# Performance work log

Hardware: AMD Instinct MI355X
Metric: run time of the kernel (lower is better)

## Reference

```python
import jax, jax.numpy as jnp
import numpy as np

NUM_DIM = 384
NUM_HEADS = 12
WIN = 7
L = WIN * WIN
NW = 4
B_ = 1024

def _relative_coords():
    ch, cw = np.meshgrid(np.arange(WIN), np.arange(WIN), indexing='ij')
    coords = np.stack([ch, cw]).reshape(2, -1)  # (2, L)
    rel = coords[:, :, None] - coords[:, None, :]  # (2, L, L)
    rel[0] += WIN - 1
    rel[1] += WIN - 1
    rel[0] *= 2 * WIN - 1
    return jnp.asarray(rel.sum(0), dtype=jnp.int32)  # (L, L)

def setup_inputs() -> dict:
    key = jax.random.key(0)
    k_x, k_m, k_qkv, k_pw, k_pb, k_rb = jax.random.split(key, 6)
    x = jax.random.normal(k_x, (B_, L, NUM_DIM), dtype=jnp.float32)
    mask = jax.random.bernoulli(k_m, 0.5, (NW, L, L))
    qkv_w = jax.random.normal(k_qkv, (3 * NUM_DIM, NUM_DIM), dtype=jnp.float32) * (NUM_DIM ** -0.5)
    proj_w = jax.random.normal(k_pw, (NUM_DIM, NUM_DIM), dtype=jnp.float32) * (NUM_DIM ** -0.5)
    proj_b = jax.random.normal(k_pb, (NUM_DIM,), dtype=jnp.float32) * 0.02
    rel_bias = jax.random.normal(k_rb, ((2 * WIN - 1) * (2 * WIN - 1), NUM_HEADS), dtype=jnp.float32) * 0.2
    rel_coords = _relative_coords()
    return {"x": x, "mask": mask, "qkv_w": qkv_w, "proj_w": proj_w,
            "proj_b": proj_b, "rel_bias": rel_bias, "rel_coords": rel_coords}

def reference(x, mask, qkv_w, proj_w, proj_b, rel_bias, rel_coords):
    Bt, Lx, C = x.shape
    H = NUM_HEADS
    hd = C // H
    scale = float(C) ** 0.5  # faithful: original multiplies by num_dim**0.5
    qkv = (x @ qkv_w.T).reshape(Bt, Lx, 3, H, hd).transpose(2, 0, 3, 1, 4)
    q, k, v = qkv[0], qkv[1], qkv[2]  # each (B_, H, L, hd)
    attn = jnp.einsum('bhqd,bhkd->bhqk', q, k) * scale
    bias = rel_bias[rel_coords].transpose(2, 0, 1)  # (H, L, L)
    attn = attn + bias[None]
    nw = mask.shape[0]
    attn = attn.reshape(-1, nw, H, Lx, Lx)
    attn = jnp.where(mask[None, :, None], jnp.float32(-100.0), attn)
    attn = attn.reshape(Bt, H, Lx, Lx)
    attn = jax.nn.softmax(attn, axis=-1)
    out = jnp.einsum('bhqk,bhkd->bhqd', attn, v)  # (B_, H, L, hd)
    out = out.transpose(0, 2, 1, 3).reshape(Bt, Lx, C)
    return out @ proj_w.T + proj_b
```

## Files before the change

kernel.cpp:

```cpp
#include <hip/hip_runtime.h>
#include <math.h>

#define NUM_B 1024
#define LW 49
#define CD 384
#define NH 12
#define HD 32
#define SCALE_F 19.595917942265423f

typedef unsigned short u16;
typedef unsigned int u32;
typedef __attribute__((ext_vector_type(8))) short short8;
typedef __attribute__((ext_vector_type(8))) _Float16 half8;
typedef __attribute__((ext_vector_type(4))) float floatx4;

#define ASM_VMCNT(n) asm volatile("s_waitcnt vmcnt(" #n ")" ::: "memory")
#define BAR()        __builtin_amdgcn_s_barrier()

static __device__ __forceinline__ u16 f2bf(float f) {
    unsigned u = __float_as_uint(f);
    u += 0x7fffu + ((u >> 16) & 1u);
    return (u16)(u >> 16);
}
static __device__ __forceinline__ float bf2f(u16 s) {
    return __uint_as_float(((unsigned)s) << 16);
}
static __device__ __forceinline__ u16 f2h_bits(float f) {
    _Float16 h = (_Float16)f;
    u16 u;
    __builtin_memcpy(&u, &h, 2);
    return u;
}
static __device__ __forceinline__ void gl_lds16(const u16* g, u16* l) {
    __builtin_amdgcn_global_load_lds(
        (const __attribute__((address_space(1))) void*)g,
        (__attribute__((address_space(3))) void*)l, 16, 0, 0);
}

#define X4 4816896
#define W4 110592
#define P4 36864
#define BM4 49152
__global__ __launch_bounds__(256) void prep(const float* __restrict__ x,
                                            const float* __restrict__ qkv_w,
                                            const float* __restrict__ proj_w,
                                            const float* __restrict__ rel_bias,
                                            const int* __restrict__ rel_coords,
                                            const int* __restrict__ mask,
                                            u16* __restrict__ xbh, u16* __restrict__ xbl,
                                            u16* __restrict__ wbh, u16* __restrict__ wbl,
                                            u16* __restrict__ pfh, u16* __restrict__ pfl,
                                            float* __restrict__ bm) {
    int idx = blockIdx.x * 256 + threadIdx.x;
    if (idx < X4) {
        float4 v = ((const float4*)x)[idx];
        ushort4 h, l;
        h.x = f2bf(v.x); l.x = f2bf(v.x - bf2f(h.x));
        h.y = f2bf(v.y); l.y = f2bf(v.y - bf2f(h.y));
        h.z = f2bf(v.z); l.z = f2bf(v.z - bf2f(h.z));
        h.w = f2bf(v.w); l.w = f2bf(v.w - bf2f(h.w));
        ((ushort4*)xbh)[idx] = h;
        ((ushort4*)xbl)[idx] = l;
    } else if (idx < X4 + W4) {
        int i = idx - X4;
        float4 v = ((const float4*)qkv_w)[i];
        ushort4 h, l;
        h.x = f2bf(v.x); l.x = f2bf(v.x - bf2f(h.x));
        h.y = f2bf(v.y); l.y = f2bf(v.y - bf2f(h.y));
        h.z = f2bf(v.z); l.z = f2bf(v.z - bf2f(h.z));
        h.w = f2bf(v.w); l.w = f2bf(v.w - bf2f(h.w));
        ((ushort4*)wbh)[i] = h;
        ((ushort4*)wbl)[i] = l;
    } else if (idx < X4 + W4 + P4) {
        int i = idx - (X4 + W4);
        float4 v = ((const float4*)proj_w)[i];
        ushort4 h, l;
        h.x = f2h_bits(v.x); l.x = f2h_bits(v.x - (float)(_Float16)v.x);
        h.y = f2h_bits(v.y); l.y = f2h_bits(v.y - (float)(_Float16)v.y);
        h.z = f2h_bits(v.z); l.z = f2h_bits(v.z - (float)(_Float16)v.z);
        h.w = f2h_bits(v.w); l.w = f2h_bits(v.w - (float)(_Float16)v.w);
        ((ushort4*)pfh)[i] = h;
        ((ushort4*)pfl)[i] = l;
    } else if (idx < X4 + W4 + P4 + BM4) {
        int t = idx - (X4 + W4 + P4);
        float4 o;
        float* op = (float*)&o;
#pragma unroll
        for (int i = 0; i < 4; ++i) {
            int j = t * 4 + i;
            int e = j & 63;
            int col = (e & 3) * 16 + (e >> 2);
            int row = (j >> 6) & 63;
            int wh_ = j >> 12;
            int w = wh_ / NH;
            int h = wh_ - w * NH;
            float val = -1.0e30f;
            if (row < LW && col < LW) {
                int ij = row * LW + col;
                val = mask[w * (LW * LW) + ij] ? -1.0e4f
                                               : rel_bias[rel_coords[ij] * NH + h];
            }
            op[i] = val;
        }
        ((float4*)bm)[t] = o;
    }
}

__global__ __launch_bounds__(256, 2) void qkv_gemm(const u16* __restrict__ Ah,
                                                   const u16* __restrict__ Al,
                                                   const u16* __restrict__ Wh,
                                                   const u16* __restrict__ Wl,
                                                   u32* __restrict__ qp,
                                                   u32* __restrict__ kp,
                                                   u16* __restrict__ vp) {
    __shared__ u16 As_h[3][128 * 32];
    __shared__ u16 Bs_h[3][128 * 32];
    __shared__ u16 As_l[2][128 * 32];
    __shared__ u16 Bs_l[2][128 * 32];
    const int tid = threadIdx.x;
    const int w = tid >> 6;
    const int lane = tid & 63;
    const int bid = blockIdx.x;
    const int logical = (bid & 7) * 441 + (bid >> 3);
    const int mt = logical / 9;
    const int nt = logical - mt * 9;
    const int m0 = mt * 128;
    const int n0 = nt * 128;
    const bool vblk = (nt >= 6);
    const int quad = lane >> 4;
    const int lc = lane & 15;
    const int wrow = (w >> 1) << 6;
    const int wcol = (w & 1) << 6;
    const int srow = lane >> 2;
    const int sch = (lane & 3) * 8;

    floatx4 acc[4][4];
#pragma unroll
    for (int a = 0; a < 4; ++a)
#pragma unroll
        for (int b = 0; b < 4; ++b) acc[a][b] = (floatx4){0.f, 0.f, 0.f, 0.f};

    auto stage_hi = [&](int buf, int k0) {
#pragma unroll
        for (int i = 0; i < 2; ++i) {
            const int rb = w * 32 + i * 16;
            gl_lds16(Ah + (size_t)(m0 + rb + srow) * CD + k0 + sch, As_h[buf] + rb * 32);
            gl_lds16(Wh + (size_t)(n0 + rb + srow) * CD + k0 + sch, Bs_h[buf] + rb * 32);
        }
    };
    auto stage_lo = [&](int buf, int k0) {
#pragma unroll
        for (int i = 0; i < 2; ++i) {
            const int rb = w * 32 + i * 16;
            gl_lds16(Al + (size_t)(m0 + rb + srow) * CD + k0 + sch, As_l[buf] + rb * 32);
            gl_lds16(Wl + (size_t)(n0 + rb + srow) * CD + k0 + sch, Bs_l[buf] + rb * 32);
        }
    };

    stage_hi(0, 0);
    if (!vblk) stage_lo(0, 0);
    stage_hi(1, 32);

#pragma unroll
    for (int t = 0; t < 12; ++t) {
        if (t == 11) { ASM_VMCNT(0); } else { ASM_VMCNT(4); }
        BAR();
        const int hb = t % 3;
        const int lb = t & 1;
        const int k0 = t * 32;
        if (!vblk) {
            if (t + 1 < 12) stage_lo((t + 1) & 1, (t + 1) * 32);
            if (t + 2 < 12) stage_hi((t + 2) % 3, (t + 2) * 32);
            short8 af_h[4], af_l[4], bf_h[4], bf_l[4];
#pragma unroll
            for (int tt = 0; tt < 4; ++tt) {
                const int ar = (wrow + tt * 16 + lc) * 32 + quad * 8;
                const int br = (wcol + tt * 16 + lc) * 32 + quad * 8;
                af_h[tt] = *(const short8*)(As_h[hb] + ar);
                af_l[tt] = *(const short8*)(As_l[lb] + ar);
                bf_h[tt] = *(const short8*)(Bs_h[hb] + br);
                bf_l[tt] = *(const short8*)(Bs_l[lb] + br);
            }
#pragma unroll
            for (int tm = 0; tm < 4; ++tm)
#pragma unroll
                for (int tn = 0; tn < 4; ++tn) {
                    acc[tm][tn] = __builtin_amdgcn_mfma_f32_16x16x32_bf16(af_h[tm], bf_h[tn], acc[tm][tn], 0, 0, 0);
                    acc[tm][tn] = __builtin_amdgcn_mfma_f32_16x16x32_bf16(af_h[tm], bf_l[tn], acc[tm][tn], 0, 0, 0);
                    acc[tm][tn] = __builtin_amdgcn_mfma_f32_16x16x32_bf16(af_l[tm], bf_h[tn], acc[tm][tn], 0, 0, 0);
                }
        } else {
            if (t + 2 < 12) stage_hi((t + 2) % 3, (t + 2) * 32);
            short8 af_h[4], bf_h[4];
#pragma unroll
            for (int tt = 0; tt < 4; ++tt) {
                af_h[tt] = *(const short8*)(As_h[hb] + (wrow + tt * 16 + lc) * 32 + quad * 8);
                bf_h[tt] = *(const short8*)(Bs_h[hb] + (wcol + tt * 16 + lc) * 32 + quad * 8);
            }
#pragma unroll
            for (int tm = 0; tm < 4; ++tm)
#pragma unroll
                for (int tn = 0; tn < 4; ++tn)
                    acc[tm][tn] = __builtin_amdgcn_mfma_f32_16x16x32_bf16(af_h[tm], bf_h[tn], acc[tm][tn], 0, 0, 0);
        }
    }

#pragma unroll
    for (int tn = 0; tn < 4; ++tn) {
        const int nst = n0 + wcol + tn * 16;
        const int t = nst / CD;
        const int rem = nst - t * CD;
        const int h = rem >> 5;
        const int db = (rem & 31) + lc;
#pragma unroll
        for (int tm = 0; tm < 4; ++tm)
#pragma unroll
            for (int r = 0; r < 4; ++r) {
                const int m = m0 + wrow + tm * 16 + quad * 4 + r;
                const int b = m / LW;
                const int l = m - b * LW;
                const size_t o = ((((size_t)b * NH + h) * LW + l) << 5) + db;
                const float vv = acc[tm][tn][r];
                if (t == 2) {
                    vp[o] = f2h_bits(vv);
                } else {
                    const unsigned bits = __float_as_uint(vv);
                    const unsigned hi_high = bits & 0xffff0000u;
                    const u16 lo = f2bf(vv - __uint_as_float(hi_high));
                    const u32 packed = hi_high | (u32)lo;
                    if (t == 0) qp[o] = packed; else kp[o] = packed;
                }
            }
    }
}

__global__ __launch_bounds__(256, 2) void proj_gemm(const u16* __restrict__ Af,
                                                    const u16* __restrict__ Wfh,
                                                    const u16* __restrict__ Wfl,
                                                    const float* __restrict__ pb,
                                                    float* __restrict__ outF) {
    __shared__ u16 As_f[3][128 * 32];
    __shared__ u16 Bs_h[3][128 * 32];
    __shared__ u16 Bs_l[2][128 * 32];
    const int tid = threadIdx.x;
    const int w = tid >> 6;
    const int lane = tid & 63;
    const int bid = blockIdx.x;
    const int logical = (bid & 7) * 147 + (bid >> 3);
    const int mt = logical / 3;
    const int nt = logical - mt * 3;
    const int m0 = mt * 128;
    const int n0 = nt * 128;
    const int quad = lane >> 4;
    const int lc = lane & 15;
    const int wrow = (w >> 1) << 6;
    const int wcol = (w & 1) << 6;
    const int srow = lane >> 2;
    const int sch = (lane & 3) * 8;

    floatx4 acc[4][4];
#pragma unroll
    for (int a = 0; a < 4; ++a)
#pragma unroll
        for (int b = 0; b < 4; ++b) acc[a][b] = (floatx4){0.f, 0.f, 0.f, 0.f};

    auto stage_hi = [&](int buf, int k0) {
#pragma unroll
        for (int i = 0; i < 2; ++i) {
            const int rb = w * 32 + i * 16;
            gl_lds16(Af + (size_t)(m0 + rb + srow) * CD + k0 + sch, As_f[buf] + rb * 32);
            gl_lds16(Wfh + (size_t)(n0 + rb + srow) * CD + k0 + sch, Bs_h[buf] + rb * 32);
        }
    };
    auto stage_lo = [&](int buf, int k0) {
#pragma unroll
        for (int i = 0; i < 2; ++i) {
            const int rb = w * 32 + i * 16;
            gl_lds16(Wfl + (size_t)(n0 + rb + srow) * CD + k0 + sch, Bs_l[buf] + rb * 32);
        }
    };

    stage_hi(0, 0);
    stage_lo(0, 0);
    stage_hi(1, 32);

#pragma unroll
    for (int t = 0; t < 12; ++t) {
        if (t == 11) { ASM_VMCNT(0); } else { ASM_VMCNT(4); }
        BAR();
        const int hb = t % 3;
        const int lb = t & 1;
        const int k0 = t * 32;
        if (t + 1 < 12) stage_lo((t + 1) & 1, (t + 1) * 32);
        if (t + 2 < 12) stage_hi((t + 2) % 3, (t + 2) * 32);
        half8 af[4], bh[4], bl[4];
#pragma unroll
        for (int tt = 0; tt < 4; ++tt) {
            const int ar = (wrow + tt * 16 + lc) * 32 + quad * 8;
            const int br = (wcol + tt * 16 + lc) * 32 + quad * 8;
            af[tt] = *(const half8*)(As_f[hb] + ar);
            bh[tt] = *(const half8*)(Bs_h[hb] + br);
            bl[tt] = *(const half8*)(Bs_l[lb] + br);
        }
#pragma unroll
        for (int tm = 0; tm < 4; ++tm)
#pragma unroll
            for (int tn = 0; tn < 4; ++tn) {
                acc[tm][tn] = __builtin_amdgcn_mfma_f32_16x16x32_f16(af[tm], bh[tn], acc[tm][tn], 0, 0, 0);
                acc[tm][tn] = __builtin_amdgcn_mfma_f32_16x16x32_f16(af[tm], bl[tn], acc[tm][tn], 0, 0, 0);
            }
    }

#pragma unroll
    for (int tn = 0; tn < 4; ++tn) {
        const int n = n0 + wcol + tn * 16 + lc;
        const float bias = pb[n];
#pragma unroll
        for (int tm = 0; tm < 4; ++tm)
#pragma unroll
            for (int r = 0; r < 4; ++r) {
                const int m = m0 + wrow + tm * 16 + quad * 4 + r;
                outF[(size_t)m * CD + n] = acc[tm][tn][r] + bias;
            }
    }
}

__global__ __launch_bounds__(64) void attn_mfma(const u32* __restrict__ qp,
                                                const u32* __restrict__ kp,
                                                const u16* __restrict__ vh,
                                                const float* __restrict__ bm,
                                                u16* __restrict__ aof) {
    const int bh = blockIdx.x;
    const int b = bh / NH;
    const int h = bh - b * NH;
    const int lane = threadIdx.x;
    const int quad = lane >> 4;
    const int lc = lane & 15;
    __shared__ u16 Vt[32 * 72];
    __shared__ u16 Ps[64 * 72];

    const size_t base = (size_t)bh * (LW * HD);

    short8 aQh[4], aQl[4], bKh[4], bKl[4];
#pragma unroll
    for (int t = 0; t < 4; ++t) {
        int row = t * 16 + lc; if (row > 48) row = 48;
        const size_t o = base + (size_t)row * HD + quad * 8;
        uint4 q0 = *(const uint4*)(qp + o);
        uint4 q1 = *(const uint4*)(qp + o + 4);
        uint4 k0 = *(const uint4*)(kp + o);
        uint4 k1 = *(const uint4*)(kp + o + 4);
        unsigned qv[8] = {q0.x, q0.y, q0.z, q0.w, q1.x, q1.y, q1.z, q1.w};
        unsigned kv[8] = {k0.x, k0.y, k0.z, k0.w, k1.x, k1.y, k1.z, k1.w};
#pragma unroll
        for (int e = 0; e < 8; ++e) {
            aQh[t][e] = (short)(qv[e] >> 16);
            aQl[t][e] = (short)(qv[e] & 0xffffu);
            bKh[t][e] = (short)(kv[e] >> 16);
            bKl[t][e] = (short)(kv[e] & 0xffffu);
        }
    }
#pragma unroll
    for (int it = 0; it < 4; ++it) {
        const int idx = lane + it * 64;
        const int j = idx >> 2;
        const int jc = j > 48 ? 48 : j;
        const int ch = (idx & 3) * 8;
        short8 vv = *(const short8*)(vh + base + (size_t)jc * HD + ch);
#pragma unroll
        for (int e = 0; e < 8; ++e) Vt[(ch + e) * 72 + j] = (u16)vv[e];
    }

    floatx4 acc[4][4];
#pragma unroll
    for (int a = 0; a < 4; ++a)
#pragma unroll
        for (int c = 0; c < 4; ++c) acc[a][c] = (floatx4){0.f, 0.f, 0.f, 0.f};
#pragma unroll
    for (int tm = 0; tm < 4; ++tm)
#pragma unroll
        for (int tn = 0; tn < 4; ++tn) {
            acc[tm][tn] = __builtin_amdgcn_mfma_f32_16x16x32_bf16(aQh[tm], bKh[tn], acc[tm][tn], 0, 0, 0);
            acc[tm][tn] = __builtin_amdgcn_mfma_f32_16x16x32_bf16(aQh[tm], bKl[tn], acc[tm][tn], 0, 0, 0);
            acc[tm][tn] = __builtin_amdgcn_mfma_f32_16x16x32_bf16(aQl[tm], bKh[tn], acc[tm][tn], 0, 0, 0);
        }

    const float* bmp = bm + (((size_t)(b & 3) * NH + h) << 12);
#pragma unroll
    for (int tm = 0; tm < 4; ++tm)
#pragma unroll
        for (int r = 0; r < 4; ++r) {
            const int row = tm * 16 + quad * 4 + r;
            const float4 bv = *(const float4*)(bmp + row * 64 + lc * 4);
            const float s0 = fmaf(acc[tm][0][r], SCALE_F, bv.x);
            const float s1 = fmaf(acc[tm][1][r], SCALE_F, bv.y);
            const float s2 = fmaf(acc[tm][2][r], SCALE_F, bv.z);
            const float s3 = fmaf(acc[tm][3][r], SCALE_F, bv.w);
            float mx = fmaxf(fmaxf(s0, s1), fmaxf(s2, s3));
#pragma unroll
            for (int off = 1; off < 16; off <<= 1) mx = fmaxf(mx, __shfl_xor(mx, off));
            const float e0 = __expf(s0 - mx);
            const float e1 = __expf(s1 - mx);
            const float e2 = __expf(s2 - mx);
            const float e3 = __expf(s3 - mx);
            float sum = (e0 + e1) + (e2 + e3);
#pragma unroll
            for (int off = 1; off < 16; off <<= 1) sum += __shfl_xor(sum, off);
            const float inv = __builtin_amdgcn_rcpf(sum);
            Ps[row * 72 +  0 + lc] = f2h_bits(e0 * inv);
            Ps[row * 72 + 16 + lc] = f2h_bits(e1 * inv);
            Ps[row * 72 + 32 + lc] = f2h_bits(e2 * inv);
            Ps[row * 72 + 48 + lc] = f2h_bits(e3 * inv);
        }

    __syncthreads();

    floatx4 o[4][2];
#pragma unroll
    for (int a = 0; a < 4; ++a) { o[a][0] = (floatx4){0.f,0.f,0.f,0.f}; o[a][1] = (floatx4){0.f,0.f,0.f,0.f}; }
#pragma unroll
    for (int ks = 0; ks < 2; ++ks) {
        const half8 bV0 = *(const half8*)(Vt + (lc) * 72 + ks * 32 + quad * 8);
        const half8 bV1 = *(const half8*)(Vt + (16 + lc) * 72 + ks * 32 + quad * 8);
#pragma unroll
        for (int tm = 0; tm < 4; ++tm) {
            const half8 aP = *(const half8*)(Ps + (tm * 16 + lc) * 72 + ks * 32 + quad * 8);
            o[tm][0] = __builtin_amdgcn_mfma_f32_16x16x32_f16(aP, bV0, o[tm][0], 0, 0, 0);
            o[tm][1] = __builtin_amdgcn_mfma_f32_16x16x32_f16(aP, bV1, o[tm][1], 0, 0, 0);
        }
    }
#pragma unroll
    for (int tm = 0; tm < 4; ++tm)
#pragma unroll
        for (int r = 0; r < 4; ++r) {
            const int i = tm * 16 + quad * 4 + r;
            if (i < LW) {
#pragma unroll
                for (int tn = 0; tn < 2; ++tn) {
                    const size_t mm = ((size_t)b * LW + i) * CD + h * HD + tn * 16 + lc;
                    aof[mm] = f2h_bits(o[tm][tn][r]);
                }
            }
        }
}

extern "C" void kernel_launch(void* const* d_in, const int* in_sizes, int n_in,
                              void* d_out, int out_size, void* d_ws, size_t ws_size,
                              hipStream_t stream) {
    const float* x          = (const float*)d_in[0];
    const int*   mask       = (const int*)d_in[1];
    const float* qkv_w      = (const float*)d_in[2];
    const float* proj_w     = (const float*)d_in[3];
    const float* proj_b     = (const float*)d_in[4];
    const float* rel_bias   = (const float*)d_in[5];
    const int*   rel_coords = (const int*)d_in[6];
    float* out = (float*)d_out;

    const size_t S = (size_t)NUM_B * NH * LW * HD;
    u16* xbh = (u16*)d_ws;
    u16* xbl = xbh + S;
    u32* kp  = (u32*)(xbl + S);
    u16* vh  = (u16*)(kp + S);
    u16* wbh = vh + S;
    u16* wbl = wbh + 442368;
    u16* pfh = wbl + 442368;
    u16* pfl = pfh + 147456;
    float* bm = (float*)(pfl + 147456);
    u32* qp = (u32*)d_out;
    u16* aof = xbh;

    prep<<<dim3(19584), dim3(256), 0, stream>>>(x, qkv_w, proj_w, rel_bias, rel_coords,
                                                mask, xbh, xbl, wbh, wbl, pfh, pfl, bm);
    qkv_gemm<<<dim3(3528), dim3(256), 0, stream>>>(xbh, xbl, wbh, wbl, qp, kp, vh);
    attn_mfma<<<dim3(NUM_B * NH), dim3(64), 0, stream>>>(qp, kp, vh, bm, aof);
    proj_gemm<<<dim3(1176), dim3(256), 0, stream>>>(aof, pfh, pfl, proj_b, out);
}
```

Measured before the change: 400.0 us.

## Shrink GEMM LDS buffering, move prefetch after compute, defer softmax normalization

In the QKV and projection GEMMs, the hi tiles drop from triple to double buffering and the lo tiles from double to single buffering. The next stages are now issued after the MFMA block behind an lgkmcnt wait and an extra barrier, and the occupancy hint of 2 is removed from launch bounds. The smaller LDS footprint may allow more resident blocks, at the cost of a second barrier per k-step and less load/compute overlap. The attention kernel now stores unnormalized exponentials in fp16 and applies the reciprocal sum to the output, which trims multiplies but changes where rounding happens.

```diff
diff --git a/kernel.cpp b/kernel.cpp
--- a/kernel.cpp
+++ b/kernel.cpp
@@ -15,6 +15,7 @@
 typedef __attribute__((ext_vector_type(4))) float floatx4;
 
 #define ASM_VMCNT(n) asm volatile("s_waitcnt vmcnt(" #n ")" ::: "memory")
+#define ASM_LGKM0()  asm volatile("s_waitcnt lgkmcnt(0)" ::: "memory")
 #define BAR()        __builtin_amdgcn_s_barrier()
 
 static __device__ __forceinline__ u16 f2bf(float f) {
@@ -106,17 +107,17 @@
     }
 }
 
-__global__ __launch_bounds__(256, 2) void qkv_gemm(const u16* __restrict__ Ah,
-                                                   const u16* __restrict__ Al,
-                                                   const u16* __restrict__ Wh,
-                                                   const u16* __restrict__ Wl,
-                                                   u32* __restrict__ qp,
-                                                   u32* __restrict__ kp,
-                                                   u16* __restrict__ vp) {
-    __shared__ u16 As_h[3][128 * 32];
-    __shared__ u16 Bs_h[3][128 * 32];
-    __shared__ u16 As_l[2][128 * 32];
-    __shared__ u16 Bs_l[2][128 * 32];
+__global__ __launch_bounds__(256) void qkv_gemm(const u16* __restrict__ Ah,
+                                                const u16* __restrict__ Al,
+                                                const u16* __restrict__ Wh,
+                                                const u16* __restrict__ Wl,
+                                                u32* __restrict__ qp,
+                                                u32* __restrict__ kp,
+                                                u16* __restrict__ vp) {
+    __shared__ u16 As_h[2][128 * 32];
+    __shared__ u16 Bs_h[2][128 * 32];
+    __shared__ u16 As_l[128 * 32];
+    __shared__ u16 Bs_l[128 * 32];
     const int tid = threadIdx.x;
     const int w = tid >> 6;
     const int lane = tid & 63;
@@ -148,38 +149,34 @@
             gl_lds16(Wh + (size_t)(n0 + rb + srow) * CD + k0 + sch, Bs_h[buf] + rb * 32);
         }
     };
-    auto stage_lo = [&](int buf, int k0) {
+    auto stage_lo = [&](int k0) {
 #pragma unroll
         for (int i = 0; i < 2; ++i) {
             const int rb = w * 32 + i * 16;
-            gl_lds16(Al + (size_t)(m0 + rb + srow) * CD + k0 + sch, As_l[buf] + rb * 32);
-            gl_lds16(Wl + (size_t)(n0 + rb + srow) * CD + k0 + sch, Bs_l[buf] + rb * 32);
+            gl_lds16(Al + (size_t)(m0 + rb + srow) * CD + k0 + sch, As_l + rb * 32);
+            gl_lds16(Wl + (size_t)(n0 + rb + srow) * CD + k0 + sch, Bs_l + rb * 32);
         }
     };
 
     stage_hi(0, 0);
-    if (!vblk) stage_lo(0, 0);
+    if (!vblk) stage_lo(0);
     stage_hi(1, 32);
 
 #pragma unroll
     for (int t = 0; t < 12; ++t) {
         if (t == 11) { ASM_VMCNT(0); } else { ASM_VMCNT(4); }
         BAR();
-        const int hb = t % 3;
-        const int lb = t & 1;
-        const int k0 = t * 32;
+        const int hb = t & 1;
         if (!vblk) {
-            if (t + 1 < 12) stage_lo((t + 1) & 1, (t + 1) * 32);
-            if (t + 2 < 12) stage_hi((t + 2) % 3, (t + 2) * 32);
             short8 af_h[4], af_l[4], bf_h[4], bf_l[4];
 #pragma unroll
             for (int tt = 0; tt < 4; ++tt) {
                 const int ar = (wrow + tt * 16 + lc) * 32 + quad * 8;
                 const int br = (wcol + tt * 16 + lc) * 32 + quad * 8;
                 af_h[tt] = *(const short8*)(As_h[hb] + ar);
-                af_l[tt] = *(const short8*)(As_l[lb] + ar);
+                af_l[tt] = *(const short8*)(As_l + ar);
                 bf_h[tt] = *(const short8*)(Bs_h[hb] + br);
-                bf_l[tt] = *(const short8*)(Bs_l[lb] + br);
+                bf_l[tt] = *(const short8*)(Bs_l + br);
             }
 #pragma unroll
             for (int tm = 0; tm < 4; ++tm)
@@ -190,7 +187,6 @@
                     acc[tm][tn] = __builtin_amdgcn_mfma_f32_16x16x32_bf16(af_l[tm], bf_h[tn], acc[tm][tn], 0, 0, 0);
                 }
         } else {
-            if (t + 2 < 12) stage_hi((t + 2) % 3, (t + 2) * 32);
             short8 af_h[4], bf_h[4];
 #pragma unroll
             for (int tt = 0; tt < 4; ++tt) {
@@ -203,6 +199,9 @@
                 for (int tn = 0; tn < 4; ++tn)
                     acc[tm][tn] = __builtin_amdgcn_mfma_f32_16x16x32_bf16(af_h[tm], bf_h[tn], acc[tm][tn], 0, 0, 0);
         }
+        ASM_LGKM0(); BAR();
+        if (!vblk && t + 1 < 12) stage_lo((t + 1) * 32);
+        if (t + 2 < 12) stage_hi(hb, (t + 2) * 32);
     }
 
 #pragma unroll
@@ -234,14 +233,14 @@
     }
 }
 
-__global__ __launch_bounds__(256, 2) void proj_gemm(const u16* __restrict__ Af,
-                                                    const u16* __restrict__ Wfh,
-                                                    const u16* __restrict__ Wfl,
-                                                    const float* __restrict__ pb,
-                                                    float* __restrict__ outF) {
-    __shared__ u16 As_f[3][128 * 32];
-    __shared__ u16 Bs_h[3][128 * 32];
-    __shared__ u16 Bs_l[2][128 * 32];
+__global__ __launch_bounds__(256) void proj_gemm(const u16* __restrict__ Af,
+                                                 const u16* __restrict__ Wfh,
+                                                 const u16* __restrict__ Wfl,
+                                                 const float* __restrict__ pb,
+                                                 float* __restrict__ outF) {
+    __shared__ u16 As_f[2][128 * 32];
+    __shared__ u16 Bs_h[2][128 * 32];
+    __shared__ u16 Bs_l[128 * 32];
     const int tid = threadIdx.x;
     const int w = tid >> 6;
     const int lane = tid & 63;
@@ -272,27 +271,23 @@
             gl_lds16(Wfh + (size_t)(n0 + rb + srow) * CD + k0 + sch, Bs_h[buf] + rb * 32);
         }
     };
-    auto stage_lo = [&](int buf, int k0) {
+    auto stage_lo = [&](int k0) {
 #pragma unroll
         for (int i = 0; i < 2; ++i) {
             const int rb = w * 32 + i * 16;
-            gl_lds16(Wfl + (size_t)(n0 + rb + srow) * CD + k0 + sch, Bs_l[buf] + rb * 32);
+            gl_lds16(Wfl + (size_t)(n0 + rb + srow) * CD + k0 + sch, Bs_l + rb * 32);
         }
     };
 
     stage_hi(0, 0);
-    stage_lo(0, 0);
+    stage_lo(0);
     stage_hi(1, 32);
 
 #pragma unroll
     for (int t = 0; t < 12; ++t) {
         if (t == 11) { ASM_VMCNT(0); } else { ASM_VMCNT(4); }
         BAR();
-        const int hb = t % 3;
-        const int lb = t & 1;
-        const int k0 = t * 32;
-        if (t + 1 < 12) stage_lo((t + 1) & 1, (t + 1) * 32);
-        if (t + 2 < 12) stage_hi((t + 2) % 3, (t + 2) * 32);
+        const int hb = t & 1;
         half8 af[4], bh[4], bl[4];
 #pragma unroll
         for (int tt = 0; tt < 4; ++tt) {
@@ -300,7 +295,7 @@
             const int br = (wcol + tt * 16 + lc) * 32 + quad * 8;
             af[tt] = *(const half8*)(As_f[hb] + ar);
             bh[tt] = *(const half8*)(Bs_h[hb] + br);
-            bl[tt] = *(const half8*)(Bs_l[lb] + br);
+            bl[tt] = *(const half8*)(Bs_l + br);
         }
 #pragma unroll
         for (int tm = 0; tm < 4; ++tm)
@@ -309,6 +304,9 @@
                 acc[tm][tn] = __builtin_amdgcn_mfma_f32_16x16x32_f16(af[tm], bh[tn], acc[tm][tn], 0, 0, 0);
                 acc[tm][tn] = __builtin_amdgcn_mfma_f32_16x16x32_f16(af[tm], bl[tn], acc[tm][tn], 0, 0, 0);
             }
+        ASM_LGKM0(); BAR();
+        if (t + 1 < 12) stage_lo((t + 1) * 32);
+        if (t + 2 < 12) stage_hi(hb, (t + 2) * 32);
     }
 
 #pragma unroll
@@ -385,6 +383,7 @@
             acc[tm][tn] = __builtin_amdgcn_mfma_f32_16x16x32_bf16(aQl[tm], bKh[tn], acc[tm][tn], 0, 0, 0);
         }
 
+    float inv_a[16];
     const float* bmp = bm + (((size_t)(b & 3) * NH + h) << 12);
 #pragma unroll
     for (int tm = 0; tm < 4; ++tm)
@@ -406,11 +405,11 @@
             float sum = (e0 + e1) + (e2 + e3);
 #pragma unroll
             for (int off = 1; off < 16; off <<= 1) sum += __shfl_xor(sum, off);
-            const float inv = __builtin_amdgcn_rcpf(sum);
-            Ps[row * 72 +  0 + lc] = f2h_bits(e0 * inv);
-            Ps[row * 72 + 16 + lc] = f2h_bits(e1 * inv);
-            Ps[row * 72 + 32 + lc] = f2h_bits(e2 * inv);
-            Ps[row * 72 + 48 + lc] = f2h_bits(e3 * inv);
+            inv_a[tm * 4 + r] = __builtin_amdgcn_rcpf(sum);
+            Ps[row * 72 +  0 + lc] = f2h_bits(e0);
+            Ps[row * 72 + 16 + lc] = f2h_bits(e1);
+            Ps[row * 72 + 32 + lc] = f2h_bits(e2);
+            Ps[row * 72 + 48 + lc] = f2h_bits(e3);
         }
 
     __syncthreads();
@@ -435,10 +434,11 @@
         for (int r = 0; r < 4; ++r) {
             const int i = tm * 16 + quad * 4 + r;
             if (i < LW) {
+                const float inv = inv_a[tm * 4 + r];
 #pragma unroll
                 for (int tn = 0; tn < 2; ++tn) {
                     const size_t mm = ((size_t)b * LW + i) * CD + h * HD + tn * 16 + lc;
-                    aof[mm] = f2h_bits(o[tm][tn][r]);
+                    aof[mm] = f2h_bits(o[tm][tn][r] * inv);
                 }
             }
         }
```

Measured after the change: 483.3 us. 1.21x slower.
